# Performance work log

Measured on AMD Instinct MI355X. Metric: run time of the kernel, lower is better.

## Reference

```python
import jax, jax.numpy as jnp
import numpy as np

EMB_DIM = 1024
B, K, N = 16, 512, 2048


def setup_inputs() -> dict:
    key0 = jax.random.key(0)
    k1, k2, k3, k4 = jax.random.split(key0, 4)
    query = jax.random.normal(k1, (K, EMB_DIM), dtype=jnp.float32)
    key = jax.random.normal(k2, (B, N, EMB_DIM), dtype=jnp.float32)
    # parameter W [emb_dim, emb_dim]; scale like kaiming-ish init
    W = jax.random.normal(k3, (EMB_DIM, EMB_DIM), dtype=jnp.float32) / np.sqrt(EMB_DIM)
    att_mask = jax.random.randint(k4, (B, K, N), 0, 2) > 0
    return {"query": query, "key": key, "W": W, "att_mask": att_mask}


def reference(query, key, W, att_mask):
    # 2D query / 3D key branch of SimpleConcatAttention, dim=-1
    d = query.shape[-1]
    # q @ W / sqrt(d): [K, d] (broadcast over batch instead of tiling)
    qW = (query @ W) / jnp.sqrt(jnp.asarray(d, query.dtype))
    # scores [b, K, N] = qW @ key^T
    att = jnp.einsum("kd,bnd->bkn", qW, key)
    att = jnp.where(att_mask, att, -jnp.inf)
    att = jax.nn.softmax(att, axis=-1)
    # out [b, K, d] = att @ key
    out = jnp.einsum("bkn,bnd->bkd", att, key)
    return out, att
```

## Files before the change

### kernel.cpp

```cpp
#include <hip/hip_runtime.h>


typedef float  f32x4  __attribute__((ext_vector_type(4)));
typedef short  bf16x8 __attribute__((ext_vector_type(8)));
typedef _Float16 f16x8 __attribute__((ext_vector_type(8)));
typedef unsigned short u16;
typedef unsigned short u16x8 __attribute__((ext_vector_type(8)));
typedef unsigned short u16x4 __attribute__((ext_vector_type(4)));

__device__ __forceinline__ void split2h(float x, u16& hi, u16& lo)
{
    _Float16 h = (_Float16)x;
    _Float16 l = (_Float16)(x - (float)h);
    hi = __builtin_bit_cast(u16, h);
    lo = __builtin_bit_cast(u16, l);
}

__device__ __forceinline__ void split2(float x, u16& hi, u16& lo)
{
    unsigned u = __float_as_uint(x);
    hi = (u16)(u >> 16);
    float hf = __uint_as_float(u & 0xFFFF0000u);
    float lf = x - hf;
    lo = (u16)(__float_as_uint(lf) >> 16);
}

__device__ __forceinline__ void async_cp16(const void* g, void* l)
{
    __builtin_amdgcn_global_load_lds(
        (const __attribute__((address_space(1))) unsigned int*)g,
        (__attribute__((address_space(3))) unsigned int*)l, 16, 0, 0);
}

__global__ __launch_bounds__(256, 2) void gemm_s(
    const u16* __restrict__ Ah, const u16* __restrict__ Al,
    const float* __restrict__ key, float* __restrict__ C)
{
    __shared__ __attribute__((aligned(16))) unsigned char smem[65536];
    u16*   Ahs = (u16*)smem;
    u16*   Als = (u16*)(smem + 16384);
    float* Bfs = (float*)(smem + 32768);

    const int tid  = threadIdx.x;
    const int lane = tid & 63;
    const int wid  = tid >> 6;
    const int wm   = wid >> 1, wn = wid & 1;
    const int fr   = lane & 15;
    const int fq   = lane >> 4;

    const int m0 = blockIdx.y * 128, n0 = blockIdx.x * 128;
    const u16*   Ag  = Ah + (long)m0 * 1024;
    const u16*   Ag2 = Al + (long)m0 * 1024;
    const float* Bg  = key + (long)blockIdx.z * 2048 * 1024 + (long)n0 * 1024;

    f32x4 acc[4][4];
#pragma unroll
    for (int i = 0; i < 4; i++)
#pragma unroll
        for (int j = 0; j < 4; j++) acc[i][j] = (f32x4){0.f, 0.f, 0.f, 0.f};

    for (int k0 = 0; k0 < 1024; k0 += 64) {
        __syncthreads();
#pragma unroll
        for (int i = 0; i < 4; i++) {
            const int q   = wid * 4 + i;
            const int p   = q * 512 + lane * 8;
            const int r   = p >> 6;
            const int oct = (p & 63) >> 3;
            const long go = (long)r * 1024 + k0 + ((oct ^ (r & 7)) << 3);
            async_cp16(Ag + go, Ahs + q * 512);
            async_cp16(Ag2 + go, Als + q * 512);
        }
#pragma unroll
        for (int i = 0; i < 8; i++) {
            const int q = wid * 8 + i;
            const int G = q * 64 + lane;
            const int r = G >> 4;
            const int g = G & 15;
            const long go = (long)r * 1024 + k0 + ((g ^ (r & 15)) << 2);
            async_cp16(Bg + go, Bfs + q * 256);
        }
        __syncthreads();

#pragma unroll
        for (int ks = 0; ks < 2; ks++) {
            const int cl = fq + ks * 4;
            f16x8 ah[4], al[4], bh[4];
#pragma unroll
            for (int i = 0; i < 4; i++) {
                const int ra = wm * 64 + i * 16 + fr;
                const int oa = ra * 64 + ((cl ^ (ra & 7)) << 3);
                ah[i] = *(const f16x8*)&Ahs[oa];
                al[i] = *(const f16x8*)&Als[oa];
                const int rb = wn * 64 + i * 16 + fr;
                const int g0 = ((2 * cl)     ^ (rb & 15)) << 2;
                const int g1 = ((2 * cl + 1) ^ (rb & 15)) << 2;
                f32x4 b0 = *(const f32x4*)&Bfs[rb * 64 + g0];
                f32x4 b1 = *(const f32x4*)&Bfs[rb * 64 + g1];
#pragma unroll
                for (int e = 0; e < 4; e++) {
                    bh[i][e]     = (_Float16)b0[e];
                    bh[i][4 + e] = (_Float16)b1[e];
                }
            }
#pragma unroll
            for (int i = 0; i < 4; i++)
#pragma unroll
                for (int j = 0; j < 4; j++) {
                    acc[i][j] = __builtin_amdgcn_mfma_f32_16x16x32_f16(ah[i], bh[j], acc[i][j], 0, 0, 0);
                    acc[i][j] = __builtin_amdgcn_mfma_f32_16x16x32_f16(al[i], bh[j], acc[i][j], 0, 0, 0);
                }
        }
    }

    float* Cg = C + (long)blockIdx.z * 512 * 2048 + (long)(m0 + wm * 64) * 2048 + (n0 + wn * 64);
    const int r4 = fq * 4;
#pragma unroll
    for (int i = 0; i < 4; i++)
#pragma unroll
        for (int j = 0; j < 4; j++) {
            float* cp = Cg + (long)(i * 16 + r4) * 2048 + j * 16 + fr;
#pragma unroll
            for (int q = 0; q < 4; q++)
                cp[(long)q * 2048] = acc[i][j][q];
        }
}

__global__ __launch_bounds__(256, 2) void gemm_nt_f16(
    const u16* __restrict__ Ah, const u16* __restrict__ Bh,
    float* __restrict__ C,
    int Kd, long sA, long sB, long sC, int ldc)
{
    constexpr int BK = 128;
    constexpr int PS = 128 * BK;
    __shared__ __attribute__((aligned(16))) u16 lds[2 * PS];
    u16* Ahs = lds;
    u16* Bhs = lds + PS;

    const int tid  = threadIdx.x;
    const int lane = tid & 63;
    const int wid  = tid >> 6;
    const int wm   = wid >> 1, wn = wid & 1;
    const int fr   = lane & 15;
    const int fq   = lane >> 4;

    const int m0 = blockIdx.y * 128, n0 = blockIdx.x * 128;
    const u16* Ag = Ah + (long)blockIdx.z * sA + (long)m0 * Kd;
    const u16* Bg = Bh + (long)blockIdx.z * sB + (long)n0 * Kd;

    f32x4 acc[4][4];
#pragma unroll
    for (int i = 0; i < 4; i++)
#pragma unroll
        for (int j = 0; j < 4; j++) acc[i][j] = (f32x4){0.f, 0.f, 0.f, 0.f};

    for (int k0 = 0; k0 < Kd; k0 += BK) {
        __syncthreads();
#pragma unroll
        for (int i = 0; i < 8; i++) {
            const int q   = wid * 8 + i;
            const int p   = q * 512 + lane * 8;
            const int r   = p / BK;
            const int oct = (p & (BK - 1)) >> 3;
            const long go = (long)r * Kd + k0 + ((oct ^ (r & 7)) << 3);
            async_cp16(Ag + go, Ahs + q * 512);
            async_cp16(Bg + go, Bhs + q * 512);
        }
        __syncthreads();

#pragma unroll
        for (int ks = 0; ks < BK / 32; ks++) {
            const int cl = fq + ks * 4;
            f16x8 ah[4], bh[4];
#pragma unroll
            for (int i = 0; i < 4; i++) {
                const int ra = wm * 64 + i * 16 + fr;
                ah[i] = *(const f16x8*)&Ahs[ra * BK + ((cl ^ (ra & 7)) << 3)];
                const int rb = wn * 64 + i * 16 + fr;
                bh[i] = *(const f16x8*)&Bhs[rb * BK + ((cl ^ (rb & 7)) << 3)];
            }
#pragma unroll
            for (int i = 0; i < 4; i++)
#pragma unroll
                for (int j = 0; j < 4; j++)
                    acc[i][j] = __builtin_amdgcn_mfma_f32_16x16x32_f16(ah[i], bh[j], acc[i][j], 0, 0, 0);
        }
    }

    float* Cg = C + (long)blockIdx.z * sC + (long)(m0 + wm * 64) * ldc + (n0 + wn * 64);
    const int r4 = fq * 4;
#pragma unroll
    for (int i = 0; i < 4; i++)
#pragma unroll
        for (int j = 0; j < 4; j++) {
            float* cp = Cg + (long)(i * 16 + r4) * ldc + j * 16 + fr;
#pragma unroll
            for (int q = 0; q < 4; q++)
                cp[(long)q * ldc] = acc[i][j][q];
        }
}

__global__ __launch_bounds__(256) void prep_all(
    const float* __restrict__ query, const float* __restrict__ W,
    const float* __restrict__ key,
    u16* __restrict__ qW_h, u16* __restrict__ qW_l, u16* __restrict__ keyT)
{
    constexpr int LDg = 72;
    __shared__ __attribute__((aligned(16))) u16 sm[4 * 64 * LDg];
    const int tid = threadIdx.x;

    if (blockIdx.x >= 128) {
        u16* t = sm;
        const int idx2 = (int)blockIdx.x - 128;
        const int bx = idx2 & 15, by = (idx2 >> 4) & 31, bz = idx2 >> 9;
        const long zin = (long)bz * 2048 * 1024;
        const int n0 = by * 64, d0 = bx * 64;
#pragma unroll
        for (int j = 0; j < 4; j++) {
            const int idx = tid + j * 256;
            const int row = idx >> 4;
            const int col = (idx & 15) * 4;
            f32x4 v = *(const f32x4*)(key + zin + (long)(n0 + row) * 1024 + d0 + col);
#pragma unroll
            for (int e = 0; e < 4; e++) {
                _Float16 hh = (_Float16)v[e];
                t[(col + e) * 65 + row] = __builtin_bit_cast(u16, hh);
            }
        }
        __syncthreads();
        const long zT = (long)bz * 1024 * 2048;
#pragma unroll
        for (int j = 0; j < 4; j++) {
            const int idx = tid + j * 256;
            const int dr = idx >> 4;
            const int nc = (idx & 15) * 4;
            u16x4 o = {t[dr * 65 + nc], t[dr * 65 + nc + 1],
                       t[dr * 65 + nc + 2], t[dr * 65 + nc + 3]};
            *(u16x4*)(keyT + zT + (long)(d0 + dr) * 2048 + n0 + nc) = o;
        }
        return;
    }

    u16* As_h = sm;
    u16* As_l = sm + 64 * LDg;
    u16* Bs_h = sm + 2 * 64 * LDg;
    u16* Bs_l = sm + 3 * 64 * LDg;

    const int lane = tid & 63, wid = tid >> 6;
    const int wm = wid >> 1, wn = wid & 1;
    const int lr = lane & 15, fq = lane >> 4;
    const int m0 = ((int)blockIdx.x >> 4) * 64;
    const int n0 = ((int)blockIdx.x & 15) * 64;
    const float* Ag = query + (long)m0 * 1024;
    const float* Bg = W + n0;

    __builtin_amdgcn_s_setprio(1);

    f32x4 acc[2][2];
#pragma unroll
    for (int i = 0; i < 2; i++)
#pragma unroll
        for (int j = 0; j < 2; j++) acc[i][j] = (f32x4){0.f, 0.f, 0.f, 0.f};

    for (int k0 = 0; k0 < 1024; k0 += 64) {
        __syncthreads();
        {
            const int row = tid >> 2, kb = (tid & 3) * 16;
            const float* src = Ag + (long)row * 1024 + k0 + kb;
            f32x4 v0 = *(const f32x4*)src;
            f32x4 v1 = *(const f32x4*)(src + 4);
            f32x4 v2 = *(const f32x4*)(src + 8);
            f32x4 v3 = *(const f32x4*)(src + 12);
            u16x8 h0, h1, l0, l1;
#pragma unroll
            for (int e = 0; e < 4; e++) {
                u16 hh, ll;
                split2h(v0[e], hh, ll); h0[e] = hh;     l0[e] = ll;
                split2h(v1[e], hh, ll); h0[4 + e] = hh; l0[4 + e] = ll;
                split2h(v2[e], hh, ll); h1[e] = hh;     l1[e] = ll;
                split2h(v3[e], hh, ll); h1[4 + e] = hh; l1[4 + e] = ll;
            }
            *(u16x8*)&As_h[row * LDg + kb]     = h0;
            *(u16x8*)&As_h[row * LDg + kb + 8] = h1;
            *(u16x8*)&As_l[row * LDg + kb]     = l0;
            *(u16x8*)&As_l[row * LDg + kb + 8] = l1;
        }
        {
            const int n = lane;
            u16x8 h0, h1, l0, l1;
#pragma unroll
            for (int kk = 0; kk < 8; kk++) {
                float x0 = Bg[(long)(k0 + wid * 16 + kk) * 1024 + n];
                float x1 = Bg[(long)(k0 + wid * 16 + 8 + kk) * 1024 + n];
                u16 hh, ll;
                split2h(x0, hh, ll); h0[kk] = hh; l0[kk] = ll;
                split2h(x1, hh, ll); h1[kk] = hh; l1[kk] = ll;
            }
            *(u16x8*)&Bs_h[n * LDg + wid * 16]     = h0;
            *(u16x8*)&Bs_h[n * LDg + wid * 16 + 8] = h1;
            *(u16x8*)&Bs_l[n * LDg + wid * 16]     = l0;
            *(u16x8*)&Bs_l[n * LDg + wid * 16 + 8] = l1;
        }
        __syncthreads();

#pragma unroll
        for (int ks = 0; ks < 2; ks++) {
            f16x8 ah[2], al[2], bh[2], bl[2];
#pragma unroll
            for (int i = 0; i < 2; i++) {
                const int ra = (wm * 32 + i * 16 + lr) * LDg + ks * 32 + fq * 8;
                ah[i] = *(const f16x8*)&As_h[ra];
                al[i] = *(const f16x8*)&As_l[ra];
                const int rb = (wn * 32 + i * 16 + lr) * LDg + ks * 32 + fq * 8;
                bh[i] = *(const f16x8*)&Bs_h[rb];
                bl[i] = *(const f16x8*)&Bs_l[rb];
            }
#pragma unroll
            for (int i = 0; i < 2; i++)
#pragma unroll
                for (int j = 0; j < 2; j++) {
                    acc[i][j] = __builtin_amdgcn_mfma_f32_16x16x32_f16(ah[i], bh[j], acc[i][j], 0, 0, 0);
                    acc[i][j] = __builtin_amdgcn_mfma_f32_16x16x32_f16(ah[i], bl[j], acc[i][j], 0, 0, 0);
                    acc[i][j] = __builtin_amdgcn_mfma_f32_16x16x32_f16(al[i], bh[j], acc[i][j], 0, 0, 0);
                }
        }
    }

    __builtin_amdgcn_s_setprio(0);

    const int r4 = fq * 4;
#pragma unroll
    for (int i = 0; i < 2; i++)
#pragma unroll
        for (int j = 0; j < 2; j++)
#pragma unroll
            for (int q = 0; q < 4; q++) {
                float v = acc[i][j][q] * (1.f / 32.f);
                u16 hh, ll;
                split2h(v, hh, ll);
                const long o = (long)(m0 + wm * 32 + i * 16 + r4 + q) * 1024
                             + n0 + wn * 32 + j * 16 + lr;
                qW_h[o] = hh;
                qW_l[o] = ll;
            }
}

template<bool BT>
__global__ __launch_bounds__(256, 2) void gemm_mfma(
    const float* __restrict__ A, const float* __restrict__ B,
    float* __restrict__ C,
    int Kd, int lda, int ldb, int ldc,
    long sA, long sB, long sC, float scale)
{
    constexpr int LD = 40;
    __shared__ __attribute__((aligned(16))) u16 As_hi[128 * LD];
    __shared__ __attribute__((aligned(16))) u16 As_lo[128 * LD];
    __shared__ __attribute__((aligned(16))) u16 Bs_hi[128 * LD];
    __shared__ __attribute__((aligned(16))) u16 Bs_lo[128 * LD];

    const int tid  = threadIdx.x;
    const int lane = tid & 63;
    const int wid  = tid >> 6;
    const int wm   = wid >> 1, wn = wid & 1;
    const int lr   = lane & 15;
    const int lk   = (lane >> 4) * 8;

    const int m0 = blockIdx.y * 128, n0 = blockIdx.x * 128;
    const float* Ag = A + (long)blockIdx.z * sA + (long)m0 * lda;
    const float* Bg = B + (long)blockIdx.z * sB + (BT ? (long)n0 * ldb : (long)n0);

    f32x4 acc[4][4];
#pragma unroll
    for (int i = 0; i < 4; i++)
#pragma unroll
        for (int j = 0; j < 4; j++) acc[i][j] = (f32x4){0.f, 0.f, 0.f, 0.f};

    for (int k0 = 0; k0 < Kd; k0 += 32) {
        __syncthreads();
#pragma unroll
        for (int it = 0; it < 2; it++) {
            const int p   = tid + it * 256;
            const int row = p >> 2, k8 = (p & 3) * 8;
            const float* src = Ag + (long)row * lda + k0 + k8;
            f32x4 v0 = *(const f32x4*)src;
            f32x4 v1 = *(const f32x4*)(src + 4);
            u16x8 h, l;
#pragma unroll
            for (int e = 0; e < 4; e++) {
                u16 hh, ll;
                split2(v0[e], hh, ll); h[e] = hh;     l[e] = ll;
                split2(v1[e], hh, ll); h[4 + e] = hh; l[4 + e] = ll;
            }
            *(u16x8*)&As_hi[row * LD + k8] = h;
            *(u16x8*)&As_lo[row * LD + k8] = l;
        }
        if constexpr (BT) {
#pragma unroll
            for (int it = 0; it < 2; it++) {
                const int p   = tid + it * 256;
                const int row = p >> 2, k8 = (p & 3) * 8;
                const float* src = Bg + (long)row * ldb + k0 + k8;
                f32x4 v0 = *(const f32x4*)src;
                f32x4 v1 = *(const f32x4*)(src + 4);
                u16x8 h, l;
#pragma unroll
                for (int e = 0; e < 4; e++) {
                    u16 hh, ll;
                    split2(v0[e], hh, ll); h[e] = hh;     l[e] = ll;
                    split2(v1[e], hh, ll); h[4 + e] = hh; l[4 + e] = ll;
                }
                *(u16x8*)&Bs_hi[row * LD + k8] = h;
                *(u16x8*)&Bs_lo[row * LD + k8] = l;
            }
        } else {
#pragma unroll
            for (int h2 = 0; h2 < 2; h2++) {
                const int n = h2 * 64 + lane;
                u16x8 h, l;
#pragma unroll
                for (int kk = 0; kk < 8; kk++) {
                    float x = Bg[(long)(k0 + wid * 8 + kk) * ldb + n];
                    u16 hh, ll;
                    split2(x, hh, ll);
                    h[kk] = hh; l[kk] = ll;
                }
                *(u16x8*)&Bs_hi[n * LD + wid * 8] = h;
                *(u16x8*)&Bs_lo[n * LD + wid * 8] = l;
            }
        }
        __syncthreads();

        bf16x8 ah[4], al[4], bh[4], bl[4];
#pragma unroll
        for (int i = 0; i < 4; i++) {
            const int ra = (wm * 64 + i * 16 + lr) * LD + lk;
            ah[i] = *(const bf16x8*)&As_hi[ra];
            al[i] = *(const bf16x8*)&As_lo[ra];
            const int rb = (wn * 64 + i * 16 + lr) * LD + lk;
            bh[i] = *(const bf16x8*)&Bs_hi[rb];
            bl[i] = *(const bf16x8*)&Bs_lo[rb];
        }
#pragma unroll
        for (int i = 0; i < 4; i++)
#pragma unroll
            for (int j = 0; j < 4; j++) {
                acc[i][j] = __builtin_amdgcn_mfma_f32_16x16x32_bf16(ah[i], bh[j], acc[i][j], 0, 0, 0);
                acc[i][j] = __builtin_amdgcn_mfma_f32_16x16x32_bf16(ah[i], bl[j], acc[i][j], 0, 0, 0);
                acc[i][j] = __builtin_amdgcn_mfma_f32_16x16x32_bf16(al[i], bh[j], acc[i][j], 0, 0, 0);
            }
    }

    float* Cg = C + (long)blockIdx.z * sC + (long)(m0 + wm * 64) * ldc + (n0 + wn * 64);
    const int r4 = (lane >> 4) * 4;
#pragma unroll
    for (int i = 0; i < 4; i++)
#pragma unroll
        for (int j = 0; j < 4; j++) {
            float* cp = Cg + (long)(i * 16 + r4) * ldc + j * 16 + lr;
#pragma unroll
            for (int q = 0; q < 4; q++)
                cp[(long)q * ldc] = acc[i][j][q] * scale;
        }
}

__global__ __launch_bounds__(256) void softmax_rows(
    float* __restrict__ att, const int* __restrict__ mask, u16* __restrict__ att_h)
{
    const int  row  = blockIdx.x;
    const int  tid  = threadIdx.x;
    const long base = (long)row * 2048 + tid * 8;

    f32x4 s0 = *(const f32x4*)(att + base);
    f32x4 s1 = *(const f32x4*)(att + base + 4);
    float x[8] = {s0[0], s0[1], s0[2], s0[3], s1[0], s1[1], s1[2], s1[3]};

    if (mask) {
        int4 mv0 = *(const int4*)(mask + base);
        int4 mv1 = *(const int4*)(mask + base + 4);
        const int mk[8] = {mv0.x, mv0.y, mv0.z, mv0.w, mv1.x, mv1.y, mv1.z, mv1.w};
#pragma unroll
        for (int j = 0; j < 8; j++) x[j] = mk[j] ? x[j] : -INFINITY;
    }

    float mx = x[0];
#pragma unroll
    for (int j = 1; j < 8; j++) mx = fmaxf(mx, x[j]);
#pragma unroll
    for (int off = 32; off > 0; off >>= 1) mx = fmaxf(mx, __shfl_down(mx, off));

    __shared__ float red[8];
    const int wave = tid >> 6, lane = tid & 63;
    if (lane == 0) red[wave] = mx;
    __syncthreads();
    mx = fmaxf(fmaxf(red[0], red[1]), fmaxf(red[2], red[3]));

    if (mx == -INFINITY) {
        f32x4 z = {0.f, 0.f, 0.f, 0.f};
        *(f32x4*)(att + base) = z;
        *(f32x4*)(att + base + 4) = z;
        if (att_h) {
            u16x8 zh = {0, 0, 0, 0, 0, 0, 0, 0};
            *(u16x8*)(att_h + base) = zh;
        }
        return;
    }

    float e[8], s = 0.f;
#pragma unroll
    for (int j = 0; j < 8; j++) { e[j] = __expf(x[j] - mx); s += e[j]; }
#pragma unroll
    for (int off = 32; off > 0; off >>= 1) s += __shfl_down(s, off);
    if (lane == 0) red[4 + wave] = s;
    __syncthreads();
    s = red[4] + red[5] + red[6] + red[7];

    const float inv = 1.f / s;
    f32x4 o0, o1;
#pragma unroll
    for (int j = 0; j < 4; j++) { o0[j] = e[j] * inv; o1[j] = e[4 + j] * inv; }
    *(f32x4*)(att + base) = o0;
    *(f32x4*)(att + base + 4) = o1;
    if (att_h) {
        u16x8 hv;
#pragma unroll
        for (int j = 0; j < 4; j++) {
            _Float16 h0 = (_Float16)o0[j];
            _Float16 h1 = (_Float16)o1[j];
            hv[j]     = __builtin_bit_cast(u16, h0);
            hv[4 + j] = __builtin_bit_cast(u16, h1);
        }
        *(u16x8*)(att_h + base) = hv;
    }
}

extern "C" void kernel_launch(void* const* d_in, const int* in_sizes, int n_in,
                              void* d_out, int out_size, void* d_ws, size_t ws_size,
                              hipStream_t stream)
{
    const float* query = nullptr;
    const float* key   = nullptr;
    const float* W     = nullptr;
    const int*   mask  = nullptr;
    for (int i = 0; i < n_in; i++) {
        switch (in_sizes[i]) {
            case 524288:   query = (const float*)d_in[i]; break;
            case 33554432: key   = (const float*)d_in[i]; break;
            case 1048576:  W     = (const float*)d_in[i]; break;
            case 16777216: mask  = (const int*)d_in[i];   break;
        }
    }

    float* out = (float*)d_out;
    float* att = out + (long)16 * 512 * 1024;

    const size_t NEED = (size_t)102760448;
    if (ws_size >= NEED) {
        char* w = (char*)d_ws;
        u16* keyT  = (u16*)(w);
        u16* att_h = (u16*)(w + 67108864);
        u16* qW_h  = (u16*)(w + 100663296);
        u16* qW_l  = (u16*)(w + 101711872);

        prep_all<<<dim3(128 + 8192), 256, 0, stream>>>(
            query, W, key, qW_h, qW_l, keyT);

        gemm_s<<<dim3(16, 4, 16), 256, 0, stream>>>(qW_h, qW_l, key, att);

        softmax_rows<<<dim3(16 * 512), 256, 0, stream>>>(att, mask, att_h);

        gemm_nt_f16<<<dim3(8, 4, 16), 256, 0, stream>>>(
            att_h, keyT, out,
            2048, (long)512 * 2048, (long)1024 * 2048, (long)512 * 1024, 1024);
    } else {
        float* qW = out;
        gemm_mfma<false><<<dim3(8, 4, 1), 256, 0, stream>>>(
            query, W, qW, 1024, 1024, 1024, 1024, 0L, 0L, 0L, 1.f / 32.f);
        gemm_mfma<true><<<dim3(16, 4, 16), 256, 0, stream>>>(
            qW, key, att, 1024, 1024, 1024, 2048,
            0L, (long)2048 * 1024, (long)512 * 2048, 1.f);
        softmax_rows<<<dim3(16 * 512), 256, 0, stream>>>(att, mask, nullptr);
        gemm_mfma<false><<<dim3(8, 4, 16), 256, 0, stream>>>(
            att, key, out, 2048, 2048, 1024, 1024,
            (long)512 * 2048, (long)2048 * 1024, (long)512 * 1024, 1.f);
    }
}
```

Before: 213.6 us.

## Fuse key fp16 transpose into attention-value GEMM, drop keyT prep pass

The separate pass that converted key to fp16 and transposed it into a workspace buffer is removed. The att@key GEMM now reads fp32 key directly, converts it to fp16 in registers, and writes the transposed, swizzled tile into LDS itself. This saves a full 128MB-read/64MB-write transform and shrinks the workspace. In exchange the GEMM does synchronous fp32 global loads (twice the bytes of the fp16 tile) plus conversion inside the main loop, with no async overlap, and each key tile is reloaded by the four M-blocks that share it. It also drops the setprio hints in the qW prep.

New measurement: 220.6 us. +3.2%, slower.

```diff
diff --git a/kernel.cpp b/kernel.cpp
--- a/kernel.cpp
+++ b/kernel.cpp
@@ -126,16 +126,14 @@
         }
 }
 
-__global__ __launch_bounds__(256, 2) void gemm_nt_f16(
-    const u16* __restrict__ Ah, const u16* __restrict__ Bh,
-    float* __restrict__ C,
-    int Kd, long sA, long sB, long sC, int ldc)
+__global__ __launch_bounds__(256, 2) void gemm_av(
+    const u16* __restrict__ Ah, const float* __restrict__ key,
+    float* __restrict__ C)
 {
     constexpr int BK = 128;
-    constexpr int PS = 128 * BK;
-    __shared__ __attribute__((aligned(16))) u16 lds[2 * PS];
+    __shared__ __attribute__((aligned(16))) u16 lds[2 * 128 * BK];
     u16* Ahs = lds;
-    u16* Bhs = lds + PS;
+    u16* Bhs = lds + 128 * BK;
 
     const int tid  = threadIdx.x;
     const int lane = tid & 63;
@@ -145,8 +143,8 @@
     const int fq   = lane >> 4;
 
     const int m0 = blockIdx.y * 128, n0 = blockIdx.x * 128;
-    const u16* Ag = Ah + (long)blockIdx.z * sA + (long)m0 * Kd;
-    const u16* Bg = Bh + (long)blockIdx.z * sB + (long)n0 * Kd;
+    const u16*   Ag = Ah + (long)blockIdx.z * 512 * 2048 + (long)m0 * 2048;
+    const float* Bg = key + (long)blockIdx.z * 2048 * 1024 + n0;
 
     f32x4 acc[4][4];
 #pragma unroll
@@ -154,22 +152,42 @@
 #pragma unroll
         for (int j = 0; j < 4; j++) acc[i][j] = (f32x4){0.f, 0.f, 0.f, 0.f};
 
-    for (int k0 = 0; k0 < Kd; k0 += BK) {
+    for (int k0 = 0; k0 < 2048; k0 += BK) {
         __syncthreads();
 #pragma unroll
         for (int i = 0; i < 8; i++) {
             const int q   = wid * 8 + i;
             const int p   = q * 512 + lane * 8;
-            const int r   = p / BK;
-            const int oct = (p & (BK - 1)) >> 3;
-            const long go = (long)r * Kd + k0 + ((oct ^ (r & 7)) << 3);
+            const int r   = p >> 7;
+            const int oct = (p & 127) >> 3;
+            const long go = (long)r * 2048 + k0 + ((oct ^ (r & 7)) << 3);
             async_cp16(Ag + go, Ahs + q * 512);
-            async_cp16(Bg + go, Bhs + q * 512);
-        }
-        __syncthreads();
-
-#pragma unroll
-        for (int ks = 0; ks < BK / 32; ks++) {
+        }
+#pragma unroll
+        for (int i = 0; i < 2; i++) {
+            const int p   = tid + i * 256;
+            const int oct = p >> 5;
+            const int d4  = (p & 31) * 4;
+            f32x4 v[8];
+#pragma unroll
+            for (int j = 0; j < 8; j++)
+                v[j] = *(const f32x4*)(Bg + (long)(k0 + oct * 8 + j) * 1024 + d4);
+#pragma unroll
+            for (int e = 0; e < 4; e++) {
+                const int d = d4 + e;
+                u16x8 hv;
+#pragma unroll
+                for (int j = 0; j < 8; j++) {
+                    _Float16 h = (_Float16)v[j][e];
+                    hv[j] = __builtin_bit_cast(u16, h);
+                }
+                *(u16x8*)&Bhs[d * BK + ((oct ^ (d & 7)) << 3)] = hv;
+            }
+        }
+        __syncthreads();
+
+#pragma unroll
+        for (int ks = 0; ks < 4; ks++) {
             const int cl = fq + ks * 4;
             f16x8 ah[4], bh[4];
 #pragma unroll
@@ -187,59 +205,26 @@
         }
     }
 
-    float* Cg = C + (long)blockIdx.z * sC + (long)(m0 + wm * 64) * ldc + (n0 + wn * 64);
+    float* Cg = C + (long)blockIdx.z * 512 * 1024 + (long)(m0 + wm * 64) * 1024 + (n0 + wn * 64);
     const int r4 = fq * 4;
 #pragma unroll
     for (int i = 0; i < 4; i++)
 #pragma unroll
         for (int j = 0; j < 4; j++) {
-            float* cp = Cg + (long)(i * 16 + r4) * ldc + j * 16 + fr;
+            float* cp = Cg + (long)(i * 16 + r4) * 1024 + j * 16 + fr;
 #pragma unroll
             for (int q = 0; q < 4; q++)
-                cp[(long)q * ldc] = acc[i][j][q];
-        }
-}
-
-__global__ __launch_bounds__(256) void prep_all(
+                cp[(long)q * 1024] = acc[i][j][q];
+        }
+}
+
+__global__ __launch_bounds__(256) void prep_qw(
     const float* __restrict__ query, const float* __restrict__ W,
-    const float* __restrict__ key,
-    u16* __restrict__ qW_h, u16* __restrict__ qW_l, u16* __restrict__ keyT)
+    u16* __restrict__ qW_h, u16* __restrict__ qW_l)
 {
     constexpr int LDg = 72;
     __shared__ __attribute__((aligned(16))) u16 sm[4 * 64 * LDg];
     const int tid = threadIdx.x;
-
-    if (blockIdx.x >= 128) {
-        u16* t = sm;
-        const int idx2 = (int)blockIdx.x - 128;
-        const int bx = idx2 & 15, by = (idx2 >> 4) & 31, bz = idx2 >> 9;
-        const long zin = (long)bz * 2048 * 1024;
-        const int n0 = by * 64, d0 = bx * 64;
-#pragma unroll
-        for (int j = 0; j < 4; j++) {
-            const int idx = tid + j * 256;
-            const int row = idx >> 4;
-            const int col = (idx & 15) * 4;
-            f32x4 v = *(const f32x4*)(key + zin + (long)(n0 + row) * 1024 + d0 + col);
-#pragma unroll
-            for (int e = 0; e < 4; e++) {
-                _Float16 hh = (_Float16)v[e];
-                t[(col + e) * 65 + row] = __builtin_bit_cast(u16, hh);
-            }
-        }
-        __syncthreads();
-        const long zT = (long)bz * 1024 * 2048;
-#pragma unroll
-        for (int j = 0; j < 4; j++) {
-            const int idx = tid + j * 256;
-            const int dr = idx >> 4;
-            const int nc = (idx & 15) * 4;
-            u16x4 o = {t[dr * 65 + nc], t[dr * 65 + nc + 1],
-                       t[dr * 65 + nc + 2], t[dr * 65 + nc + 3]};
-            *(u16x4*)(keyT + zT + (long)(d0 + dr) * 2048 + n0 + nc) = o;
-        }
-        return;
-    }
 
     u16* As_h = sm;
     u16* As_l = sm + 64 * LDg;
@@ -253,8 +238,6 @@
     const int n0 = ((int)blockIdx.x & 15) * 64;
     const float* Ag = query + (long)m0 * 1024;
     const float* Bg = W + n0;
-
-    __builtin_amdgcn_s_setprio(1);
 
     f32x4 acc[2][2];
 #pragma unroll
@@ -325,8 +308,6 @@
                 }
         }
     }
-
-    __builtin_amdgcn_s_setprio(0);
 
     const int r4 = fq * 4;
 #pragma unroll
@@ -553,24 +534,20 @@
     float* out = (float*)d_out;
     float* att = out + (long)16 * 512 * 1024;
 
-    const size_t NEED = (size_t)102760448;
+    const size_t NEED = (size_t)35651584;
     if (ws_size >= NEED) {
         char* w = (char*)d_ws;
-        u16* keyT  = (u16*)(w);
-        u16* att_h = (u16*)(w + 67108864);
-        u16* qW_h  = (u16*)(w + 100663296);
-        u16* qW_l  = (u16*)(w + 101711872);
-
-        prep_all<<<dim3(128 + 8192), 256, 0, stream>>>(
-            query, W, key, qW_h, qW_l, keyT);
+        u16* att_h = (u16*)(w);
+        u16* qW_h  = (u16*)(w + 33554432);
+        u16* qW_l  = (u16*)(w + 34603008);
+
+        prep_qw<<<dim3(128), 256, 0, stream>>>(query, W, qW_h, qW_l);
 
         gemm_s<<<dim3(16, 4, 16), 256, 0, stream>>>(qW_h, qW_l, key, att);
 
         softmax_rows<<<dim3(16 * 512), 256, 0, stream>>>(att, mask, att_h);
 
-        gemm_nt_f16<<<dim3(8, 4, 16), 256, 0, stream>>>(
-            att_h, keyT, out,
-            2048, (long)512 * 2048, (long)1024 * 2048, (long)512 * 1024, 1024);
+        gemm_av<<<dim3(8, 4, 16), 256, 0, stream>>>(att_h, key, out);
     } else {
         float* qW = out;
         gemm_mfma<false><<<dim3(8, 4, 1), 256, 0, stream>>>(
```
